# Kernel optimization log

Measured on AMD Instinct MI355X. Metric: run time of the kernel, lower is better.

The kernel has to match this reference:

```python
import jax, jax.numpy as jnp
import numpy as np

N_NODES = 50000
N_EDGES = 200000
IN_DIM = 512
HID = 2000
LAT = 128


def setup_inputs() -> dict:
    key = jax.random.key(0)
    ks = jax.random.split(key, 6)
    x = jax.random.normal(ks[0], (N_NODES, IN_DIM), dtype=jnp.float32)
    edge_index = jax.random.randint(ks[1], (2, N_EDGES), 0, N_NODES, dtype=jnp.int64)
    # glorot-ish scales so ReLU/Sigmoid stay in a sane range
    W1 = jax.random.normal(ks[2], (IN_DIM, HID), dtype=jnp.float32) * (1.0 / np.sqrt(IN_DIM))
    b1 = jnp.zeros((HID,), dtype=jnp.float32)
    W2 = jax.random.normal(ks[3], (HID, LAT), dtype=jnp.float32) * (1.0 / np.sqrt(HID))
    b2 = jnp.zeros((LAT,), dtype=jnp.float32)
    return {"x": x, "edge_index": edge_index, "W1": W1, "b1": b1, "W2": W2, "b2": b2}


def gcn_conv(x, edge_index, W, b):
    """PyG GCNConv: D^-1/2 (A+I) D^-1/2 (X W) + b, unit edge weights."""
    n = x.shape[0]
    loops = jnp.arange(n, dtype=edge_index.dtype)
    row = jnp.concatenate([edge_index[0], loops])  # source nodes
    col = jnp.concatenate([edge_index[1], loops])  # target nodes
    deg = jax.ops.segment_sum(jnp.ones_like(col, dtype=x.dtype), col, num_segments=n)
    dis = jnp.where(deg > 0, jax.lax.rsqrt(deg), 0.0)  # deg^-1/2, inf -> 0
    norm = dis[row] * dis[col]                         # [E+N]
    h = x @ W                                          # transform first: [N, out]
    msg = h[row] * norm[:, None]                       # gather + normalize: [E+N, out]
    out = jax.ops.segment_sum(msg, col, num_segments=n)  # scatter-add
    return out + b


def reference(x, edge_index, W1, b1, W2, b2):
    h = jax.nn.relu(gcn_conv(x, edge_index, W1, b1))
    return jax.nn.sigmoid(gcn_conv(h, edge_index, W2, b2))
```

## Files before the change

kernel.cpp:

```cpp
#include <hip/hip_runtime.h>
#include <hip/hip_fp16.h>

#define NN 50000
#define NE 200000
#define IND 512
#define HIDD 2000
#define LATD 128

#define M_PAD 50176
#define N1_PAD 2048
#define MT1 392
#define SLAB1 49
#define NBLK 196

typedef _Float16 f16x8 __attribute__((ext_vector_type(8)));
typedef float f32x4 __attribute__((ext_vector_type(4)));

__device__ __forceinline__ void gload_lds16(const _Float16* g, _Float16* l) {
    __builtin_amdgcn_global_load_lds(
        (const __attribute__((address_space(1))) unsigned int*)g,
        (__attribute__((address_space(3))) unsigned int*)l,
        16, 0, 0);
}

__global__ void k_degree(const int* __restrict__ col, int* __restrict__ deg) {
    int e = blockIdx.x * 256 + threadIdx.x;
    if (e < NE) atomicAdd(&deg[col[e]], 1);
}

__global__ void k_dis(const int* __restrict__ deg, float* __restrict__ dis) {
    int i = blockIdx.x * 256 + threadIdx.x;
    if (i < NN) dis[i] = rsqrtf((float)deg[i] + 1.0f);
}

__global__ void k_bsum(const int* __restrict__ deg, int* __restrict__ bsum) {
    __shared__ int sm[4];
    int i = blockIdx.x * 256 + threadIdx.x;
    int v = (i < NN) ? deg[i] : 0;
    #pragma unroll
    for (int off = 32; off; off >>= 1) v += __shfl_down(v, off, 64);
    if ((threadIdx.x & 63) == 0) sm[threadIdx.x >> 6] = v;
    __syncthreads();
    if (threadIdx.x == 0) bsum[blockIdx.x] = sm[0] + sm[1] + sm[2] + sm[3];
}

__global__ void k_bscan(int* __restrict__ bsum) {
    __shared__ int sm[256];
    int tid = threadIdx.x;
    int v = (tid < NBLK) ? bsum[tid] : 0;
    sm[tid] = v;
    __syncthreads();
    #pragma unroll
    for (int off = 1; off < 256; off <<= 1) {
        int t = (tid >= off) ? sm[tid - off] : 0;
        __syncthreads();
        sm[tid] += t;
        __syncthreads();
    }
    if (tid < NBLK) bsum[tid] = sm[tid] - v;
}

__global__ void k_scan_final(const int* __restrict__ deg, const int* __restrict__ bsum,
                             int* __restrict__ row_ptr) {
    __shared__ int sm[256];
    int b = blockIdx.x, tid = threadIdx.x;
    int i = b * 256 + tid;
    int v = (i < NN) ? deg[i] : 0;
    sm[tid] = v;
    __syncthreads();
    #pragma unroll
    for (int off = 1; off < 256; off <<= 1) {
        int t = (tid >= off) ? sm[tid - off] : 0;
        __syncthreads();
        sm[tid] += t;
        __syncthreads();
    }
    if (i < NN) row_ptr[i] = bsum[b] + sm[tid] - v;
    if (i == NN - 1) row_ptr[NN] = bsum[b] + sm[tid];
}

__global__ void k_fill(const int* __restrict__ ei, const int* __restrict__ row_ptr,
                       int* __restrict__ cursor, int* __restrict__ csr_src) {
    int e = blockIdx.x * 256 + threadIdx.x;
    if (e < NE) {
        int r = ei[e], c = ei[NE + e];
        int pos = atomicAdd(&cursor[c], 1);
        csr_src[row_ptr[c] + pos] = r;
    }
}

__global__ void k_transpose_tiled(const float* __restrict__ in,
                                  _Float16* __restrict__ out, int R, int C, int ldo) {
    __shared__ float sm[32][33];
    int c0 = blockIdx.x * 32, r0 = blockIdx.y * 32;
    int tx = threadIdx.x & 31, ty = threadIdx.x >> 5;
    #pragma unroll
    for (int i = 0; i < 4; ++i) {
        int r = r0 + ty + i * 8, c = c0 + tx;
        sm[ty + i * 8][tx] = (r < R && c < C) ? in[(size_t)r * C + c] : 0.f;
    }
    __syncthreads();
    #pragma unroll
    for (int i = 0; i < 4; ++i) {
        int c = c0 + ty + i * 8, r = r0 + tx;
        if (c < C && r < R) out[(size_t)c * ldo + r] = (_Float16)sm[tx][ty + i * 8];
    }
}

__global__ void k_xcvt(const float* __restrict__ in, _Float16* __restrict__ out, int n8) {
    int i = blockIdx.x * 256 + threadIdx.x;
    if (i < n8) {
        float4 a = ((const float4*)in)[i * 2];
        float4 b = ((const float4*)in)[i * 2 + 1];
        f16x8 o;
        o[0] = (_Float16)a.x; o[1] = (_Float16)a.y; o[2] = (_Float16)a.z; o[3] = (_Float16)a.w;
        o[4] = (_Float16)b.x; o[5] = (_Float16)b.y; o[6] = (_Float16)b.z; o[7] = (_Float16)b.w;
        ((f16x8*)out)[i] = o;
    }
}

__global__ void k_gather_x(const _Float16* __restrict__ xh, const int* __restrict__ row_ptr,
                           const int* __restrict__ csr_src, const float* __restrict__ dis,
                           _Float16* __restrict__ Ah) {
    int dst = blockIdx.x * 4 + (threadIdx.x >> 6);
    if (dst >= NN) return;
    int lane = threadIdx.x & 63;
    float dd = dis[dst];
    const f16x8* vb = (const f16x8*)xh;
    f16x8 sv = vb[(size_t)dst * 64 + lane];
    float acc[8];
    #pragma unroll
    for (int q = 0; q < 8; ++q) acc[q] = dd * (float)sv[q];
    int beg = row_ptr[dst], end = row_ptr[dst + 1];
    for (int c = beg; c < end; c += 64) {
        int n = end - c; if (n > 64) n = 64;
        int li = (lane < n) ? csr_src[c + lane] : 0;
        float lns = (lane < n) ? dis[li] : 0.f;
        int s0 = __shfl(li, 0);
        f16x8 vnext = vb[(size_t)s0 * 64 + lane];
        for (int j = 0; j < n; ++j) {
            f16x8 v = vnext;
            if (j + 1 < n) {
                int s1 = __shfl(li, j + 1);
                vnext = vb[(size_t)s1 * 64 + lane];
            }
            float ns = __shfl(lns, j);
            #pragma unroll
            for (int q = 0; q < 8; ++q) acc[q] += ns * (float)v[q];
        }
    }
    f16x8 o;
    #pragma unroll
    for (int q = 0; q < 8; ++q) o[q] = (_Float16)(dd * acc[q]);
    *(f16x8*)(Ah + (size_t)dst * IND + lane * 8) = o;
}

__global__ void k_gather_t(const float* __restrict__ t, const int* __restrict__ row_ptr,
                           const int* __restrict__ csr_src, const float* __restrict__ dis,
                           const float* __restrict__ b2, float* __restrict__ out) {
    int dst = blockIdx.x * 4 + (threadIdx.x >> 6);
    if (dst >= NN) return;
    int lane = threadIdx.x & 63;
    float dd = dis[dst];
    const float2* vb = (const float2*)t;
    float2 td = vb[(size_t)dst * 64 + lane];
    float accx = dd * td.x, accy = dd * td.y;
    int beg = row_ptr[dst], end = row_ptr[dst + 1];
    for (int c = beg; c < end; c += 64) {
        int n = end - c; if (n > 64) n = 64;
        int li = (lane < n) ? csr_src[c + lane] : 0;
        float lns = (lane < n) ? dis[li] : 0.f;
        int s0 = __shfl(li, 0);
        float2 vnext = vb[(size_t)s0 * 64 + lane];
        for (int j = 0; j < n; ++j) {
            float2 v = vnext;
            if (j + 1 < n) {
                int s1 = __shfl(li, j + 1);
                vnext = vb[(size_t)s1 * 64 + lane];
            }
            float ns = __shfl(lns, j);
            accx += ns * v.x; accy += ns * v.y;
        }
    }
    float2 bb = *(const float2*)(b2 + lane * 2);
    float vx = dd * accx + bb.x;
    float vy = dd * accy + bb.y;
    float2 o;
    o.x = 1.0f / (1.0f + __expf(-vx));
    o.y = 1.0f / (1.0f + __expf(-vy));
    *(float2*)(out + (size_t)dst * LATD + lane * 2) = o;
}

__global__ __launch_bounds__(256, 2) void k_gemm1(
    const _Float16* __restrict__ A,
    const _Float16* __restrict__ Bt,
    const float* __restrict__ bias,
    _Float16* __restrict__ Ch)
{
    const int b = blockIdx.x;
    const int mT = (b & 7) * SLAB1 + ((b >> 3) >> 4);
    const int nT = (b >> 3) & 15;
    const int mBase = mT * 128;
    const int nBase = nT * 128;

    __shared__ __align__(16) _Float16 As[2 * 128 * 32];
    __shared__ __align__(16) _Float16 Bs[2 * 128 * 32];

    const int tid = threadIdx.x;
    const int lane = tid & 63;
    const int w = tid >> 6;

    const int srow = w * 32 + (lane >> 2);
    const int scol = (lane & 3) * 8;
    const _Float16* Ag0 = A + (size_t)(mBase + srow) * IND + scol;
    const _Float16* Ag1 = Ag0 + (size_t)16 * IND;
    const _Float16* Bg0 = Bt + (size_t)(nBase + srow) * IND + scol;
    const _Float16* Bg1 = Bg0 + (size_t)16 * IND;

    const int wm = (w >> 1) * 64;
    const int wn = (w & 1) * 64;
    const int lm = lane & 15;
    const int quad = lane >> 4;

    f32x4 acc[4][4];
    #pragma unroll
    for (int i = 0; i < 4; ++i)
        #pragma unroll
        for (int j = 0; j < 4; ++j)
            acc[i][j] = (f32x4){0.f, 0.f, 0.f, 0.f};

    for (int k0 = 0; k0 < IND; k0 += 64) {
        #pragma unroll
        for (int s = 0; s < 2; ++s) {
            gload_lds16(Ag0 + k0 + s * 32, As + s * 4096 + w * 1024);
            gload_lds16(Ag1 + k0 + s * 32, As + s * 4096 + w * 1024 + 512);
            gload_lds16(Bg0 + k0 + s * 32, Bs + s * 4096 + w * 1024);
            gload_lds16(Bg1 + k0 + s * 32, Bs + s * 4096 + w * 1024 + 512);
        }
        __syncthreads();

        #pragma unroll
        for (int s = 0; s < 2; ++s) {
            f16x8 af[4], bfr[4];
            #pragma unroll
            for (int mi = 0; mi < 4; ++mi)
                af[mi] = *(const f16x8*)&As[s * 4096 + (wm + mi * 16 + lm) * 32 + quad * 8];
            #pragma unroll
            for (int ni = 0; ni < 4; ++ni)
                bfr[ni] = *(const f16x8*)&Bs[s * 4096 + (wn + ni * 16 + lm) * 32 + quad * 8];
            #pragma unroll
            for (int mi = 0; mi < 4; ++mi)
                #pragma unroll
                for (int ni = 0; ni < 4; ++ni)
                    acc[mi][ni] = __builtin_amdgcn_mfma_f32_16x16x32_f16(
                        af[mi], bfr[ni], acc[mi][ni], 0, 0, 0);
        }
        __syncthreads();
    }

    #pragma unroll
    for (int mi = 0; mi < 4; ++mi) {
        #pragma unroll
        for (int ni = 0; ni < 4; ++ni) {
            int col = nBase + wn + ni * 16 + lm;
            float bval = bias[col];
            #pragma unroll
            for (int r = 0; r < 4; ++r) {
                int rowg = mBase + wm + mi * 16 + quad * 4 + r;
                float v = fmaxf(acc[mi][ni][r] + bval, 0.f);
                Ch[(size_t)rowg * N1_PAD + col] = (_Float16)v;
            }
        }
    }
}

__global__ __launch_bounds__(256, 2) void k_gemm2(
    const _Float16* __restrict__ A,
    const _Float16* __restrict__ Bt,
    float* __restrict__ Cf)
{
    __shared__ __align__(16) _Float16 As[2 * 64 * 32];
    __shared__ __align__(16) _Float16 Bs[2 * 128 * 32];

    const int tid = threadIdx.x;
    const int lane = tid & 63;
    const int w = tid >> 6;
    const int mBase = blockIdx.x * 64;

    const int srA = w * 16 + (lane >> 2);
    const int srB = w * 32 + (lane >> 2);
    const int scol = (lane & 3) * 8;
    const _Float16* Ag  = A + (size_t)(mBase + srA) * N1_PAD + scol;
    const _Float16* Bg0 = Bt + (size_t)srB * N1_PAD + scol;
    const _Float16* Bg1 = Bg0 + (size_t)16 * N1_PAD;

    const int wm = (w & 1) * 32;
    const int wn = (w >> 1) * 64;
    const int lm = lane & 15;
    const int quad = lane >> 4;

    f32x4 acc[2][4];
    #pragma unroll
    for (int i = 0; i < 2; ++i)
        #pragma unroll
        for (int j = 0; j < 4; ++j)
            acc[i][j] = (f32x4){0.f, 0.f, 0.f, 0.f};

    for (int k0 = 0; k0 < N1_PAD; k0 += 64) {
        #pragma unroll
        for (int s = 0; s < 2; ++s) {
            gload_lds16(Ag + k0 + s * 32, As + s * 2048 + w * 512);
            gload_lds16(Bg0 + k0 + s * 32, Bs + s * 4096 + w * 1024);
            gload_lds16(Bg1 + k0 + s * 32, Bs + s * 4096 + w * 1024 + 512);
        }
        __syncthreads();

        #pragma unroll
        for (int s = 0; s < 2; ++s) {
            f16x8 af[2], bfr[4];
            #pragma unroll
            for (int mi = 0; mi < 2; ++mi)
                af[mi] = *(const f16x8*)&As[s * 2048 + (wm + mi * 16 + lm) * 32 + quad * 8];
            #pragma unroll
            for (int ni = 0; ni < 4; ++ni)
                bfr[ni] = *(const f16x8*)&Bs[s * 4096 + (wn + ni * 16 + lm) * 32 + quad * 8];
            #pragma unroll
            for (int mi = 0; mi < 2; ++mi)
                #pragma unroll
                for (int ni = 0; ni < 4; ++ni)
                    acc[mi][ni] = __builtin_amdgcn_mfma_f32_16x16x32_f16(
                        af[mi], bfr[ni], acc[mi][ni], 0, 0, 0);
        }
        __syncthreads();
    }

    #pragma unroll
    for (int mi = 0; mi < 2; ++mi) {
        #pragma unroll
        for (int ni = 0; ni < 4; ++ni) {
            int col = wn + ni * 16 + lm;
            #pragma unroll
            for (int r = 0; r < 4; ++r) {
                int rowg = mBase + wm + mi * 16 + quad * 4 + r;
                Cf[(size_t)rowg * LATD + col] = acc[mi][ni][r];
            }
        }
    }
}

extern "C" void kernel_launch(void* const* d_in, const int* in_sizes, int n_in,
                              void* d_out, int out_size, void* d_ws, size_t ws_size,
                              hipStream_t stream) {
    const float* x  = (const float*)d_in[0];
    const int* ei   = (const int*)d_in[1];
    const float* W1 = (const float*)d_in[2];
    const float* b1 = (const float*)d_in[3];
    const float* W2 = (const float*)d_in[4];
    const float* b2 = (const float*)d_in[5];
    float* out = (float*)d_out;

    char* p = (char*)d_ws;
    auto alloc = [&](size_t bytes) {
        char* q = p; p += (bytes + 255) & ~(size_t)255; return q;
    };
    int* deg        = (int*)alloc((size_t)NN * 4);
    int* bsum       = (int*)alloc((size_t)NBLK * 4);
    int* row_ptr    = (int*)alloc((size_t)(NN + 1) * 4);
    int* cursor     = (int*)alloc((size_t)NN * 4);
    int* csr_src    = (int*)alloc((size_t)NE * 4);
    float* dis      = (float*)alloc((size_t)NN * 4);
    float* b1pad    = (float*)alloc((size_t)N1_PAD * 4);
    _Float16* W1T   = (_Float16*)alloc((size_t)N1_PAD * IND * 2);
    _Float16* W2T   = (_Float16*)alloc((size_t)LATD * N1_PAD * 2);
    _Float16* xh    = (_Float16*)alloc((size_t)NN * IND * 2);
    _Float16* Ah    = (_Float16*)alloc((size_t)M_PAD * IND * 2);
    _Float16* h     = (_Float16*)alloc((size_t)M_PAD * N1_PAD * 2);
    float* t        = (float*)alloc((size_t)M_PAD * LATD * 4);

    hipMemsetAsync(deg,    0, (size_t)NN * 4, stream);
    hipMemsetAsync(cursor, 0, (size_t)NN * 4, stream);
    hipMemsetAsync(b1pad,  0, (size_t)N1_PAD * 4, stream);
    hipMemsetAsync(W1T,    0, (size_t)N1_PAD * IND * 2, stream);
    hipMemsetAsync(W2T,    0, (size_t)LATD * N1_PAD * 2, stream);
    hipMemcpyAsync(b1pad, b1, (size_t)HIDD * 4, hipMemcpyDeviceToDevice, stream);

    k_degree<<<(NE + 255) / 256, 256, 0, stream>>>(ei + NE, deg);
    k_dis<<<(NN + 255) / 256, 256, 0, stream>>>(deg, dis);
    k_bsum<<<NBLK, 256, 0, stream>>>(deg, bsum);
    k_bscan<<<1, 256, 0, stream>>>(bsum);
    k_scan_final<<<NBLK, 256, 0, stream>>>(deg, bsum, row_ptr);
    k_fill<<<(NE + 255) / 256, 256, 0, stream>>>(ei, row_ptr, cursor, csr_src);

    {
        dim3 gt1((HIDD + 31) / 32, (IND + 31) / 32);
        k_transpose_tiled<<<gt1, 256, 0, stream>>>(W1, W1T, IND, HIDD, IND);
        dim3 gt2((LATD + 31) / 32, (HIDD + 31) / 32);
        k_transpose_tiled<<<gt2, 256, 0, stream>>>(W2, W2T, HIDD, LATD, N1_PAD);
        k_xcvt<<<(NN * IND / 8 + 255) / 256, 256, 0, stream>>>(x, xh, NN * IND / 8);
    }

    k_gather_x<<<(NN + 3) / 4, 256, 0, stream>>>(xh, row_ptr, csr_src, dis, Ah);

    k_gemm1<<<8 * SLAB1 * 16, 256, 0, stream>>>(Ah, W1T, b1pad, h);
    k_gemm2<<<M_PAD / 64, 256, 0, stream>>>(h, W2T, t);

    k_gather_t<<<(NN + 3) / 4, 256, 0, stream>>>(t, row_ptr, csr_src, dis, b2, out);
}
```

Baseline: 499.6 us.

## Batch neighbor gathers four at a time and split GEMM1 into two launches

Both CSR gather kernels now issue four independent neighbor row loads per iteration, with clamped indices and zeroed weights past the end, in place of a one-ahead software prefetch. The aim is more memory-level parallelism on the latency-bound random gathers. GEMM1 now takes an M-tile offset and slab size and is launched twice (25 and 24 slabs), changing how tiles map across the XCDs and how the tail wave is handled, at the cost of one extra launch. Clamped duplicate loads add some redundant traffic on short neighbor lists.

Result: no change. 503.0 us (+0.7%).

```diff
diff --git a/kernel.cpp b/kernel.cpp
--- a/kernel.cpp
+++ b/kernel.cpp
@@ -10,7 +10,6 @@
 #define M_PAD 50176
 #define N1_PAD 2048
 #define MT1 392
-#define SLAB1 49
 #define NBLK 196
 
 typedef _Float16 f16x8 __attribute__((ext_vector_type(8)));
@@ -136,17 +135,24 @@
         int n = end - c; if (n > 64) n = 64;
         int li = (lane < n) ? csr_src[c + lane] : 0;
         float lns = (lane < n) ? dis[li] : 0.f;
-        int s0 = __shfl(li, 0);
-        f16x8 vnext = vb[(size_t)s0 * 64 + lane];
-        for (int j = 0; j < n; ++j) {
-            f16x8 v = vnext;
-            if (j + 1 < n) {
-                int s1 = __shfl(li, j + 1);
-                vnext = vb[(size_t)s1 * 64 + lane];
-            }
-            float ns = __shfl(lns, j);
-            #pragma unroll
-            for (int q = 0; q < 8; ++q) acc[q] += ns * (float)v[q];
+        for (int j = 0; j < n; j += 4) {
+            int j1 = j + 1 < n ? j + 1 : n - 1;
+            int j2 = j + 2 < n ? j + 2 : n - 1;
+            int j3 = j + 3 < n ? j + 3 : n - 1;
+            int s0 = __shfl(li, j),  s1 = __shfl(li, j1);
+            int s2 = __shfl(li, j2), s3 = __shfl(li, j3);
+            float w0 = __shfl(lns, j);
+            float w1 = (j + 1 < n) ? __shfl(lns, j1) : 0.f;
+            float w2 = (j + 2 < n) ? __shfl(lns, j2) : 0.f;
+            float w3 = (j + 3 < n) ? __shfl(lns, j3) : 0.f;
+            f16x8 v0 = vb[(size_t)s0 * 64 + lane];
+            f16x8 v1 = vb[(size_t)s1 * 64 + lane];
+            f16x8 v2 = vb[(size_t)s2 * 64 + lane];
+            f16x8 v3 = vb[(size_t)s3 * 64 + lane];
+            #pragma unroll
+            for (int q = 0; q < 8; ++q)
+                acc[q] += w0 * (float)v0[q] + w1 * (float)v1[q]
+                        + w2 * (float)v2[q] + w3 * (float)v3[q];
         }
     }
     f16x8 o;
@@ -170,16 +176,22 @@
         int n = end - c; if (n > 64) n = 64;
         int li = (lane < n) ? csr_src[c + lane] : 0;
         float lns = (lane < n) ? dis[li] : 0.f;
-        int s0 = __shfl(li, 0);
-        float2 vnext = vb[(size_t)s0 * 64 + lane];
-        for (int j = 0; j < n; ++j) {
-            float2 v = vnext;
-            if (j + 1 < n) {
-                int s1 = __shfl(li, j + 1);
-                vnext = vb[(size_t)s1 * 64 + lane];
-            }
-            float ns = __shfl(lns, j);
-            accx += ns * v.x; accy += ns * v.y;
+        for (int j = 0; j < n; j += 4) {
+            int j1 = j + 1 < n ? j + 1 : n - 1;
+            int j2 = j + 2 < n ? j + 2 : n - 1;
+            int j3 = j + 3 < n ? j + 3 : n - 1;
+            int s0 = __shfl(li, j),  s1 = __shfl(li, j1);
+            int s2 = __shfl(li, j2), s3 = __shfl(li, j3);
+            float w0 = __shfl(lns, j);
+            float w1 = (j + 1 < n) ? __shfl(lns, j1) : 0.f;
+            float w2 = (j + 2 < n) ? __shfl(lns, j2) : 0.f;
+            float w3 = (j + 3 < n) ? __shfl(lns, j3) : 0.f;
+            float2 v0 = vb[(size_t)s0 * 64 + lane];
+            float2 v1 = vb[(size_t)s1 * 64 + lane];
+            float2 v2 = vb[(size_t)s2 * 64 + lane];
+            float2 v3 = vb[(size_t)s3 * 64 + lane];
+            accx += w0 * v0.x + w1 * v1.x + w2 * v2.x + w3 * v3.x;
+            accy += w0 * v0.y + w1 * v1.y + w2 * v2.y + w3 * v3.y;
         }
     }
     float2 bb = *(const float2*)(b2 + lane * 2);
@@ -195,10 +207,11 @@
     const _Float16* __restrict__ A,
     const _Float16* __restrict__ Bt,
     const float* __restrict__ bias,
-    _Float16* __restrict__ Ch)
+    _Float16* __restrict__ Ch,
+    int mT0, int slab)
 {
     const int b = blockIdx.x;
-    const int mT = (b & 7) * SLAB1 + ((b >> 3) >> 4);
+    const int mT = mT0 + (b & 7) * slab + ((b >> 3) >> 4);
     const int nT = (b >> 3) & 15;
     const int mBase = mT * 128;
     const int nBase = nT * 128;
@@ -401,7 +414,8 @@
 
     k_gather_x<<<(NN + 3) / 4, 256, 0, stream>>>(xh, row_ptr, csr_src, dis, Ah);
 
-    k_gemm1<<<8 * SLAB1 * 16, 256, 0, stream>>>(Ah, W1T, b1pad, h);
+    k_gemm1<<<8 * 25 * 16, 256, 0, stream>>>(Ah, W1T, b1pad, h, 0, 25);
+    k_gemm1<<<8 * 24 * 16, 256, 0, stream>>>(Ah, W1T, b1pad, h, 200, 24);
     k_gemm2<<<M_PAD / 64, 256, 0, stream>>>(h, W2T, t);
 
     k_gather_t<<<(NN + 3) / 4, 256, 0, stream>>>(t, row_ptr, csr_src, dis, b2, out);
```
